# Performance work log

Measured on AMD Instinct MI355X. Metric: run time of the kernel, lower is better.

Reference implementation:

```python
import jax, jax.numpy as jnp
import numpy as np

B, T, C, H = 4, 4096, 1024, 128

def setup_inputs() -> dict:
    key = jax.random.key(0)
    k1, k2, k3, k4 = jax.random.split(key, 4)
    x = jax.random.normal(k1, (B, T, C), dtype=jnp.float32)
    # nn.Linear(embed, head, bias=False): y = x @ W, store W as [C, H]
    s = 1.0 / np.sqrt(C)
    Wk = jax.random.normal(k2, (C, H), dtype=jnp.float32) * s
    Wq = jax.random.normal(k3, (C, H), dtype=jnp.float32) * s
    Wv = jax.random.normal(k4, (C, H), dtype=jnp.float32) * s
    return {"x": x, "Wk": Wk, "Wq": Wq, "Wv": Wv}

def reference(x, Wk, Wq, Wv):
    Bx, Tx, Cx = x.shape
    scale = Wk.shape[1] ** -0.5
    k = x @ Wk  # [B,T,H]
    q = x @ Wq
    v = x @ Wv
    att = jnp.einsum('bth,bsh->bts', q, k) * scale  # [B,T,T]
    causal = jnp.triu(jnp.ones((Tx, Tx), dtype=bool), k=1)
    att = jnp.where(causal, -jnp.inf, att)
    att = jax.nn.softmax(att, axis=-1)
    # dropout is identity in eval mode
    out = jnp.einsum('bts,bsh->bth', att, v)  # [B,T,H]
    return out
```

## Files before the change

kernel.cpp:

```cpp
#include <hip/hip_runtime.h>
#include <stdint.h>
#include <math.h>

#define B_ 4
#define T_ 4096
#define C_ 1024
#define H_ 128

typedef __attribute__((ext_vector_type(8))) short s16x8;
typedef __attribute__((ext_vector_type(4))) float f32x4;

__device__ __forceinline__ unsigned short f2bf(float f) {
    union { float f; unsigned u; } v; v.f = f;
    unsigned r = v.u + 0x7fffu + ((v.u >> 16) & 1u);
    return (unsigned short)(r >> 16);
}

__device__ __forceinline__ s16x8 as_frag(uint4 u) {
    union { uint4 u; s16x8 s; } v; v.u = u; return v.s;
}

#define QSC (0.0883883476f * 1.4426950408f)

__global__ __launch_bounds__(256) void k_wt(const float* __restrict__ Wk,
                                            const float* __restrict__ Wq,
                                            const float* __restrict__ Wv,
                                            unsigned short* __restrict__ Wt) {
    __shared__ float tile[64][65];
    int w = blockIdx.z;
    const float* W = (w == 0) ? Wk : (w == 1) ? Wq : Wv;
    int c0 = blockIdx.x * 64, h0 = blockIdx.y * 64;
    int tid = threadIdx.x;
#pragma unroll
    for (int k = 0; k < 16; k++) {
        int idx = tid + k * 256;
        int r = idx >> 6, c = idx & 63;
        tile[r][c] = W[(size_t)(c0 + r) * H_ + h0 + c];
    }
    __syncthreads();
#pragma unroll
    for (int k = 0; k < 16; k++) {
        int idx = tid + k * 256;
        int hh = idx >> 6, cc = idx & 63;
        Wt[(size_t)(w * H_ + h0 + hh) * C_ + c0 + cc] = f2bf(tile[cc][hh]);
    }
}

__global__ __launch_bounds__(256, 3) void k_qkv(const float* __restrict__ x,
                                                const unsigned short* __restrict__ Wt,
                                                unsigned short* __restrict__ Qb,
                                                unsigned short* __restrict__ Kb,
                                                unsigned short* __restrict__ Vt) {
    __shared__ unsigned short a_lds[2][64 * 72];
    int tid = threadIdx.x;
    int wv = tid >> 6, lane = tid & 63, quad = lane >> 4, lo = lane & 15;
    int r0 = blockIdx.x * 64;
    int cb = blockIdx.y;
    int nt0 = wv * 3;

    f32x4 acc[3][4];
#pragma unroll
    for (int i = 0; i < 3; i++)
#pragma unroll
        for (int j = 0; j < 4; j++) acc[i][j] = (f32x4){0.f, 0.f, 0.f, 0.f};

    const int row_s = tid >> 2;
    const int seg_s = (tid & 3) * 16;
    size_t xbase = (size_t)(r0 + row_s) * C_ + seg_s;

    const unsigned short* wp[3];
#pragma unroll
    for (int nt = 0; nt < 3; nt++)
        wp[nt] = Wt + (size_t)(cb * 192 + (nt0 + nt) * 16 + lo) * C_ + quad * 8;

    auto pack_store = [&](unsigned short* buf, const float4 (&f)[4]) {
        uint4 u0, u1;
        u0.x = (unsigned)f2bf(f[0].x) | ((unsigned)f2bf(f[0].y) << 16);
        u0.y = (unsigned)f2bf(f[0].z) | ((unsigned)f2bf(f[0].w) << 16);
        u0.z = (unsigned)f2bf(f[1].x) | ((unsigned)f2bf(f[1].y) << 16);
        u0.w = (unsigned)f2bf(f[1].z) | ((unsigned)f2bf(f[1].w) << 16);
        u1.x = (unsigned)f2bf(f[2].x) | ((unsigned)f2bf(f[2].y) << 16);
        u1.y = (unsigned)f2bf(f[2].z) | ((unsigned)f2bf(f[2].w) << 16);
        u1.z = (unsigned)f2bf(f[3].x) | ((unsigned)f2bf(f[3].y) << 16);
        u1.w = (unsigned)f2bf(f[3].z) | ((unsigned)f2bf(f[3].w) << 16);
        *(uint4*)&buf[row_s * 72 + seg_s] = u0;
        *(uint4*)&buf[row_s * 72 + seg_s + 8] = u1;
    };
    auto load_x = [&](float4 (&f)[4], int kc) {
        const float* xp = x + xbase + kc * 64;
#pragma unroll
        for (int j = 0; j < 4; j++) f[j] = *(const float4*)(xp + j * 4);
    };

    float4 xr[4];
    load_x(xr, 0);
    pack_store(a_lds[0], xr);
    __syncthreads();

    for (int kc = 0; kc < 16; kc++) {
        const unsigned short* buf = a_lds[kc & 1];
        float4 xn[4];
        if (kc < 15) load_x(xn, kc + 1);
        s16x8 b[3][2];
#pragma unroll
        for (int nt = 0; nt < 3; nt++)
#pragma unroll
            for (int kh = 0; kh < 2; kh++)
                b[nt][kh] = *(const s16x8*)(wp[nt] + kc * 64 + kh * 32);
        s16x8 af[4][2];
#pragma unroll
        for (int mt = 0; mt < 4; mt++)
#pragma unroll
            for (int kh = 0; kh < 2; kh++)
                af[mt][kh] = *(const s16x8*)&buf[(mt * 16 + lo) * 72 + kh * 32 + quad * 8];
#pragma unroll
        for (int nt = 0; nt < 3; nt++)
#pragma unroll
            for (int kh = 0; kh < 2; kh++)
#pragma unroll
                for (int mt = 0; mt < 4; mt++)
                    acc[nt][mt] = __builtin_amdgcn_mfma_f32_16x16x32_bf16(
                        af[mt][kh], b[nt][kh], acc[nt][mt], 0, 0, 0);
        if (kc < 15) pack_store((unsigned short*)a_lds[(kc & 1) ^ 1], xn);
        __syncthreads();
    }

#pragma unroll
    for (int nt = 0; nt < 3; nt++) {
        int col = cb * 192 + (nt0 + nt) * 16 + lo;
        int w = col >> 7, h = col & 127;
#pragma unroll
        for (int mt = 0; mt < 4; mt++) {
            int mrow = r0 + mt * 16 + quad * 4;
            if (w == 2) {
                int b = mrow >> 12, t0 = mrow & 4095;
                int tp = (t0 & ~31) + (((t0 & 15) >> 2) << 3) + (((t0 >> 4) & 1) << 2);
                uint2 pk;
                pk.x = (unsigned)f2bf(acc[nt][mt][0]) | ((unsigned)f2bf(acc[nt][mt][1]) << 16);
                pk.y = (unsigned)f2bf(acc[nt][mt][2]) | ((unsigned)f2bf(acc[nt][mt][3]) << 16);
                *(uint2*)(Vt + (size_t)(b * H_ + h) * T_ + tp) = pk;
            } else if (w == 1) {
                unsigned short* dst = Qb + (size_t)mrow * H_ + h;
#pragma unroll
                for (int r = 0; r < 4; r++)
                    dst[(size_t)r * H_] = f2bf(acc[nt][mt][r] * QSC);
            } else {
                unsigned short* dst = Kb + (size_t)mrow * H_ + h;
#pragma unroll
                for (int r = 0; r < 4; r++)
                    dst[(size_t)r * H_] = f2bf(acc[nt][mt][r]);
            }
        }
    }
}

#define LOAD_KV(kv0)                                                            \
    do {                                                                        \
        const uint4* kg = (const uint4*)(Kb + (size_t)(batch * T_ + (kv0) + srow_k) * H_); \
        pk0 = kg[sseg_k + 0]; pk1 = kg[sseg_k + 1];                             \
        pk2 = kg[sseg_k + 2]; pk3 = kg[sseg_k + 3];                             \
        const uint4* vg = (const uint4*)(Vt + (size_t)(batch * H_ + srow_v) * T_ + (kv0)); \
        pv0 = vg[sseg_v + 0]; pv1 = vg[sseg_v + 1];                             \
        pv2 = vg[sseg_v + 2]; pv3 = vg[sseg_v + 3];                             \
    } while (0)

template <int NSPLIT>
__global__ __launch_bounds__(256, 3) void k_attn(const unsigned short* __restrict__ Qb,
                                                 const unsigned short* __restrict__ Kb,
                                                 const unsigned short* __restrict__ Vt,
                                                 float* __restrict__ Opart,
                                                 float* __restrict__ Mpart,
                                                 float* __restrict__ Lpart,
                                                 float* __restrict__ out) {
    __shared__ uint4 kbuf[64 * 16];
    __shared__ uint4 vbuf[128 * 8];

    int tid = threadIdx.x;
    int wv = tid >> 6, lane = tid & 63, quad = lane >> 4, lo = lane & 15;

    int id = blockIdx.x;
    int qt = 63 - id / (4 * NSPLIT);
    int rem = id % (4 * NSPLIT);
    int batch = rem / NSPLIT;
    int split = rem % NSPLIT;
    int m0 = qt * 64 + wv * 16;
    int query = m0 + lo;

    s16x8 qf[4];
    size_t qrow = (size_t)(batch * T_ + m0 + lo) * H_;
#pragma unroll
    for (int ks = 0; ks < 4; ks++)
        qf[ks] = *(const s16x8*)(Qb + qrow + ks * 32 + quad * 8);

    f32x4 acc_o[8];
#pragma unroll
    for (int o = 0; o < 8; o++) acc_o[o] = (f32x4){0.f, 0.f, 0.f, 0.f};
    float m_i = -INFINITY, l_i = 0.f;

    const int srow_k = tid >> 2, sseg_k = (tid & 3) * 4;
    const int srow_v = tid >> 1, sseg_v = (tid & 1) * 4;

    uint4 pk0, pk1, pk2, pk3, pv0, pv1, pv2, pv3;
    if (split <= qt) LOAD_KV(split * 64);

    for (int t = split; t <= qt; t += NSPLIT) {
        int kv0 = t * 64;
        kbuf[srow_k * 16 + ((sseg_k + 0) ^ (srow_k & 15))] = pk0;
        kbuf[srow_k * 16 + ((sseg_k + 1) ^ (srow_k & 15))] = pk1;
        kbuf[srow_k * 16 + ((sseg_k + 2) ^ (srow_k & 15))] = pk2;
        kbuf[srow_k * 16 + ((sseg_k + 3) ^ (srow_k & 15))] = pk3;
        vbuf[srow_v * 8 + ((sseg_v + 0) ^ (srow_v & 7))] = pv0;
        vbuf[srow_v * 8 + ((sseg_v + 1) ^ (srow_v & 7))] = pv1;
        vbuf[srow_v * 8 + ((sseg_v + 2) ^ (srow_v & 7))] = pv2;
        vbuf[srow_v * 8 + ((sseg_v + 3) ^ (srow_v & 7))] = pv3;
        __syncthreads();
        if (t + NSPLIT <= qt) LOAD_KV((t + NSPLIT) * 64);

        f32x4 s_acc[4];
#pragma unroll
        for (int nt = 0; nt < 4; nt++) s_acc[nt] = (f32x4){0.f, 0.f, 0.f, 0.f};
#pragma unroll
        for (int ks = 0; ks < 4; ks++) {
#pragma unroll
            for (int nt = 0; nt < 4; nt++) {
                s16x8 kf = as_frag(kbuf[(nt * 16 + lo) * 16 + ((ks * 4 + quad) ^ lo)]);
                s_acc[nt] = __builtin_amdgcn_mfma_f32_16x16x32_bf16(kf, qf[ks], s_acc[nt], 0, 0, 0);
            }
        }

        float p[4][4];
        bool diag = (t == qt);
#pragma unroll
        for (int nt = 0; nt < 4; nt++)
#pragma unroll
            for (int r = 0; r < 4; r++) {
                float sv = s_acc[nt][r];
                if (diag && (kv0 + nt * 16 + quad * 4 + r > query)) sv = -INFINITY;
                p[nt][r] = sv;
            }

        float mx = p[0][0];
#pragma unroll
        for (int nt = 0; nt < 4; nt++)
#pragma unroll
            for (int r = 0; r < 4; r++) mx = fmaxf(mx, p[nt][r]);
        mx = fmaxf(mx, __shfl_xor(mx, 16));
        mx = fmaxf(mx, __shfl_xor(mx, 32));
        float mnew = fmaxf(m_i, mx);
        if (__any(mnew > m_i)) {
            float alpha = exp2f(m_i - mnew);
            l_i *= alpha;
            m_i = mnew;
#pragma unroll
            for (int o = 0; o < 8; o++)
#pragma unroll
                for (int r = 0; r < 4; r++) acc_o[o][r] *= alpha;
        }
        float rs = 0.f;
#pragma unroll
        for (int nt = 0; nt < 4; nt++)
#pragma unroll
            for (int r = 0; r < 4; r++) {
                float pv = exp2f(p[nt][r] - mnew);
                p[nt][r] = pv;
                rs += pv;
            }
        rs += __shfl_xor(rs, 16);
        rs += __shfl_xor(rs, 32);
        l_i += rs;

        s16x8 pf[2];
#pragma unroll
        for (int kt = 0; kt < 2; kt++) {
            uint4 u;
            u.x = (__float_as_uint(p[2 * kt][0]) >> 16) | ((__float_as_uint(p[2 * kt][1]) >> 16) << 16);
            u.y = (__float_as_uint(p[2 * kt][2]) >> 16) | ((__float_as_uint(p[2 * kt][3]) >> 16) << 16);
            u.z = (__float_as_uint(p[2 * kt + 1][0]) >> 16) | ((__float_as_uint(p[2 * kt + 1][1]) >> 16) << 16);
            u.w = (__float_as_uint(p[2 * kt + 1][2]) >> 16) | ((__float_as_uint(p[2 * kt + 1][3]) >> 16) << 16);
            pf[kt] = as_frag(u);
        }

#pragma unroll
        for (int kt = 0; kt < 2; kt++)
#pragma unroll
            for (int o = 0; o < 8; o++) {
                int vrow = o * 16 + lo;
                s16x8 vf = as_frag(vbuf[vrow * 8 + ((kt * 4 + quad) ^ (vrow & 7))]);
                acc_o[o] = __builtin_amdgcn_mfma_f32_16x16x32_bf16(vf, pf[kt], acc_o[o], 0, 0, 0);
            }
        __syncthreads();
    }

    int rowg = batch * T_ + m0 + lo;
    if (NSPLIT == 1) {
        float inv = 1.0f / l_i;
#pragma unroll
        for (int o = 0; o < 8; o++) {
            float4 v = {acc_o[o][0] * inv, acc_o[o][1] * inv,
                        acc_o[o][2] * inv, acc_o[o][3] * inv};
            *(float4*)(out + (size_t)rowg * H_ + o * 16 + quad * 4) = v;
        }
    } else {
        float* Op = Opart + (size_t)split * (16384 * 128);
#pragma unroll
        for (int o = 0; o < 8; o++) {
            float4 v = {acc_o[o][0], acc_o[o][1], acc_o[o][2], acc_o[o][3]};
            *(float4*)(Op + (size_t)rowg * H_ + o * 16 + quad * 4) = v;
        }
        if (quad == 0) {
            Mpart[split * 16384 + rowg] = m_i;
            Lpart[split * 16384 + rowg] = l_i;
        }
    }
}

template <int NSPLIT>
__global__ __launch_bounds__(256) void k_comb(const float* __restrict__ Opart,
                                              const float* __restrict__ Mpart,
                                              const float* __restrict__ Lpart,
                                              float* __restrict__ out) {
    int tid = threadIdx.x;
    int row = blockIdx.x * 8 + (tid >> 5);
    int h4 = (tid & 31) * 4;
    float m[NSPLIT], l[NSPLIT];
    float M = -INFINITY;
#pragma unroll
    for (int s = 0; s < NSPLIT; s++) {
        m[s] = Mpart[s * 16384 + row];
        l[s] = Lpart[s * 16384 + row];
        M = fmaxf(M, m[s]);
    }
    float4 o = {0.f, 0.f, 0.f, 0.f};
    float den = 0.f;
#pragma unroll
    for (int s = 0; s < NSPLIT; s++) {
        float w = exp2f(m[s] - M);
        den += w * l[s];
        float4 v = *(const float4*)(Opart + ((size_t)s * 16384 + row) * H_ + h4);
        o.x += w * v.x; o.y += w * v.y; o.z += w * v.z; o.w += w * v.w;
    }
    float inv = 1.0f / den;
    float4 r = {o.x * inv, o.y * inv, o.z * inv, o.w * inv};
    *(float4*)(out + (size_t)row * H_ + h4) = r;
}

extern "C" void kernel_launch(void* const* d_in, const int* in_sizes, int n_in,
                              void* d_out, int out_size, void* d_ws, size_t ws_size,
                              hipStream_t stream) {
    const float* x  = (const float*)d_in[0];
    const float* Wk = (const float*)d_in[1];
    const float* Wq = (const float*)d_in[2];
    const float* Wv = (const float*)d_in[3];
    char* ws = (char*)d_ws;
    unsigned short* Wt = (unsigned short*)ws;
    unsigned short* Qb = (unsigned short*)(ws + (1u << 20));
    unsigned short* Kb = (unsigned short*)(ws + (5u << 20));
    unsigned short* Vt = (unsigned short*)(ws + (9u << 20));
    float* out = (float*)d_out;

    const size_t SPLIT_O = (size_t)16384 * 128 * 4;
    const size_t base = (size_t)13 << 20;
    const size_t need4 = base + 4 * SPLIT_O + 8 * 65536;
    const size_t need2 = base + 2 * SPLIT_O + 4 * 65536;

    k_wt  <<<dim3(16, 2, 3), 256, 0, stream>>>(Wk, Wq, Wv, Wt);
    k_qkv <<<dim3(256, 2), 256, 0, stream>>>(x, Wt, Qb, Kb, Vt);

    if (ws_size >= need4) {
        float* Op = (float*)(ws + base);
        float* Mp = (float*)(ws + base + 4 * SPLIT_O);
        float* Lp = (float*)(ws + base + 4 * SPLIT_O + 4 * 65536);
        k_attn<4><<<1024, 256, 0, stream>>>(Qb, Kb, Vt, Op, Mp, Lp, out);
        k_comb<4><<<2048, 256, 0, stream>>>(Op, Mp, Lp, out);
    } else if (ws_size >= need2) {
        float* Op = (float*)(ws + base);
        float* Mp = (float*)(ws + base + 2 * SPLIT_O);
        float* Lp = (float*)(ws + base + 2 * SPLIT_O + 2 * 65536);
        k_attn<2><<<512, 256, 0, stream>>>(Qb, Kb, Vt, Op, Mp, Lp, out);
        k_comb<2><<<2048, 256, 0, stream>>>(Op, Mp, Lp, out);
    } else {
        k_attn<1><<<256, 256, 0, stream>>>(Qb, Kb, Vt, nullptr, nullptr, nullptr, out);
    }
}
```

Before: 168.0 us.

## Split causal attention into contiguous KV chunks, lazy rescale, retile QKV projection

Attention work is now split into contiguous chunks of at most CH key tiles per query tile, replacing the strided NSPLIT split. This balances block work across the causal triangle, and the combine kernel merges a variable number of partials per row. The online softmax now rescales only when the row max grows by more than 8 (log2 units) and defers the cross-lane row-sum reduction to the end, which cuts shuffles and rescale work per tile. The QKV projection uses 512-thread blocks over 32 rows covering all 384 columns, with a two-stage unrolled double buffer. The trade-offs are larger partial workspace and combine traffic, and the lazy rescale threshold could in principle affect numerical range.

```diff
diff --git a/kernel.cpp b/kernel.cpp
--- a/kernel.cpp
+++ b/kernel.cpp
@@ -18,6 +18,11 @@
 
 __device__ __forceinline__ s16x8 as_frag(uint4 u) {
     union { uint4 u; s16x8 s; } v; v.u = u; return v.s;
+}
+
+__host__ __device__ constexpr int chunks_total(int CH) {
+    int a = 64 / CH, b = 64 % CH;
+    return CH * a * (a + 1) / 2 + b * (a + 1);
 }
 
 #define QSC (0.0883883476f * 1.4426950408f)
@@ -46,70 +51,50 @@
     }
 }
 
-__global__ __launch_bounds__(256, 3) void k_qkv(const float* __restrict__ x,
+__global__ __launch_bounds__(512, 4) void k_qkv(const float* __restrict__ x,
                                                 const unsigned short* __restrict__ Wt,
                                                 unsigned short* __restrict__ Qb,
                                                 unsigned short* __restrict__ Kb,
                                                 unsigned short* __restrict__ Vt) {
-    __shared__ unsigned short a_lds[2][64 * 72];
+    __shared__ unsigned short a_lds[2][32 * 72];
     int tid = threadIdx.x;
     int wv = tid >> 6, lane = tid & 63, quad = lane >> 4, lo = lane & 15;
-    int r0 = blockIdx.x * 64;
-    int cb = blockIdx.y;
-    int nt0 = wv * 3;
-
-    f32x4 acc[3][4];
+    int r0 = blockIdx.x * 32;
+
+    f32x4 acc[3][2];
 #pragma unroll
     for (int i = 0; i < 3; i++)
 #pragma unroll
-        for (int j = 0; j < 4; j++) acc[i][j] = (f32x4){0.f, 0.f, 0.f, 0.f};
-
-    const int row_s = tid >> 2;
-    const int seg_s = (tid & 3) * 16;
+        for (int j = 0; j < 2; j++) acc[i][j] = (f32x4){0.f, 0.f, 0.f, 0.f};
+
+    const int row_s = tid >> 4;
+    const int seg_s = (tid & 15) * 4;
     size_t xbase = (size_t)(r0 + row_s) * C_ + seg_s;
 
     const unsigned short* wp[3];
 #pragma unroll
     for (int nt = 0; nt < 3; nt++)
-        wp[nt] = Wt + (size_t)(cb * 192 + (nt0 + nt) * 16 + lo) * C_ + quad * 8;
-
-    auto pack_store = [&](unsigned short* buf, const float4 (&f)[4]) {
-        uint4 u0, u1;
-        u0.x = (unsigned)f2bf(f[0].x) | ((unsigned)f2bf(f[0].y) << 16);
-        u0.y = (unsigned)f2bf(f[0].z) | ((unsigned)f2bf(f[0].w) << 16);
-        u0.z = (unsigned)f2bf(f[1].x) | ((unsigned)f2bf(f[1].y) << 16);
-        u0.w = (unsigned)f2bf(f[1].z) | ((unsigned)f2bf(f[1].w) << 16);
-        u1.x = (unsigned)f2bf(f[2].x) | ((unsigned)f2bf(f[2].y) << 16);
-        u1.y = (unsigned)f2bf(f[2].z) | ((unsigned)f2bf(f[2].w) << 16);
-        u1.z = (unsigned)f2bf(f[3].x) | ((unsigned)f2bf(f[3].y) << 16);
-        u1.w = (unsigned)f2bf(f[3].z) | ((unsigned)f2bf(f[3].w) << 16);
-        *(uint4*)&buf[row_s * 72 + seg_s] = u0;
-        *(uint4*)&buf[row_s * 72 + seg_s + 8] = u1;
+        wp[nt] = Wt + (size_t)((wv * 3 + nt) * 16 + lo) * C_ + quad * 8;
+
+    auto load_x = [&](int kc) -> float4 {
+        return *(const float4*)(x + xbase + kc * 64);
     };
-    auto load_x = [&](float4 (&f)[4], int kc) {
-        const float* xp = x + xbase + kc * 64;
-#pragma unroll
-        for (int j = 0; j < 4; j++) f[j] = *(const float4*)(xp + j * 4);
+    auto pack_store = [&](unsigned short* buf, float4 f) {
+        uint2 u;
+        u.x = (unsigned)f2bf(f.x) | ((unsigned)f2bf(f.y) << 16);
+        u.y = (unsigned)f2bf(f.z) | ((unsigned)f2bf(f.w) << 16);
+        *(uint2*)&buf[row_s * 72 + seg_s] = u;
     };
-
-    float4 xr[4];
-    load_x(xr, 0);
-    pack_store(a_lds[0], xr);
-    __syncthreads();
-
-    for (int kc = 0; kc < 16; kc++) {
-        const unsigned short* buf = a_lds[kc & 1];
-        float4 xn[4];
-        if (kc < 15) load_x(xn, kc + 1);
+    auto compute = [&](const unsigned short* buf, int kc) {
         s16x8 b[3][2];
 #pragma unroll
         for (int nt = 0; nt < 3; nt++)
 #pragma unroll
             for (int kh = 0; kh < 2; kh++)
                 b[nt][kh] = *(const s16x8*)(wp[nt] + kc * 64 + kh * 32);
-        s16x8 af[4][2];
-#pragma unroll
-        for (int mt = 0; mt < 4; mt++)
+        s16x8 af[2][2];
+#pragma unroll
+        for (int mt = 0; mt < 2; mt++)
 #pragma unroll
             for (int kh = 0; kh < 2; kh++)
                 af[mt][kh] = *(const s16x8*)&buf[(mt * 16 + lo) * 72 + kh * 32 + quad * 8];
@@ -118,19 +103,34 @@
 #pragma unroll
             for (int kh = 0; kh < 2; kh++)
 #pragma unroll
-                for (int mt = 0; mt < 4; mt++)
+                for (int mt = 0; mt < 2; mt++)
                     acc[nt][mt] = __builtin_amdgcn_mfma_f32_16x16x32_bf16(
                         af[mt][kh], b[nt][kh], acc[nt][mt], 0, 0, 0);
-        if (kc < 15) pack_store((unsigned short*)a_lds[(kc & 1) ^ 1], xn);
+    };
+
+    float4 p0 = load_x(0);
+    float4 p1 = load_x(1);
+    pack_store(a_lds[0], p0);
+    __syncthreads();
+
+    for (int kc2 = 0; kc2 < 8; kc2++) {
+        int kc = kc2 * 2;
+        if (kc + 2 < 16) p0 = load_x(kc + 2);
+        compute(a_lds[0], kc);
+        pack_store(a_lds[1], p1);
         __syncthreads();
+        if (kc + 3 < 16) p1 = load_x(kc + 3);
+        compute(a_lds[1], kc + 1);
+        if (kc + 2 < 16) pack_store(a_lds[0], p0);
+        __syncthreads();
     }
 
 #pragma unroll
     for (int nt = 0; nt < 3; nt++) {
-        int col = cb * 192 + (nt0 + nt) * 16 + lo;
+        int col = (wv * 3 + nt) * 16 + lo;
         int w = col >> 7, h = col & 127;
 #pragma unroll
-        for (int mt = 0; mt < 4; mt++) {
+        for (int mt = 0; mt < 2; mt++) {
             int mrow = r0 + mt * 16 + quad * 4;
             if (w == 2) {
                 int b = mrow >> 12, t0 = mrow & 4095;
@@ -164,7 +164,7 @@
         pv2 = vg[sseg_v + 2]; pv3 = vg[sseg_v + 3];                             \
     } while (0)
 
-template <int NSPLIT>
+template <int CH>
 __global__ __launch_bounds__(256, 3) void k_attn(const unsigned short* __restrict__ Qb,
                                                  const unsigned short* __restrict__ Kb,
                                                  const unsigned short* __restrict__ Vt,
@@ -179,10 +179,18 @@
     int wv = tid >> 6, lane = tid & 63, quad = lane >> 4, lo = lane & 15;
 
     int id = blockIdx.x;
-    int qt = 63 - id / (4 * NSPLIT);
-    int rem = id % (4 * NSPLIT);
-    int batch = rem / NSPLIT;
-    int split = rem % NSPLIT;
+    int qt, batch, tbeg, tend, slot = 0;
+    if constexpr (CH > 0) {
+        slot = id >> 2; batch = id & 3;
+        int s = slot, q = 63;
+        for (;;) { int nc = (q + CH) / CH; if (s < nc) break; s -= nc; --q; }
+        qt = q;
+        tbeg = s * CH;
+        tend = min(tbeg + CH, qt + 1);
+    } else {
+        qt = 63 - (id >> 2); batch = id & 3;
+        tbeg = 0; tend = qt + 1;
+    }
     int m0 = qt * 64 + wv * 16;
     int query = m0 + lo;
 
@@ -201,9 +209,9 @@
     const int srow_v = tid >> 1, sseg_v = (tid & 1) * 4;
 
     uint4 pk0, pk1, pk2, pk3, pv0, pv1, pv2, pv3;
-    if (split <= qt) LOAD_KV(split * 64);
-
-    for (int t = split; t <= qt; t += NSPLIT) {
+    LOAD_KV(tbeg * 64);
+
+    for (int t = tbeg; t < tend; ++t) {
         int kv0 = t * 64;
         kbuf[srow_k * 16 + ((sseg_k + 0) ^ (srow_k & 15))] = pk0;
         kbuf[srow_k * 16 + ((sseg_k + 1) ^ (srow_k & 15))] = pk1;
@@ -214,7 +222,7 @@
         vbuf[srow_v * 8 + ((sseg_v + 2) ^ (srow_v & 7))] = pv2;
         vbuf[srow_v * 8 + ((sseg_v + 3) ^ (srow_v & 7))] = pv3;
         __syncthreads();
-        if (t + NSPLIT <= qt) LOAD_KV((t + NSPLIT) * 64);
+        if (t + 1 < tend) LOAD_KV((t + 1) * 64);
 
         f32x4 s_acc[4];
 #pragma unroll
@@ -244,10 +252,10 @@
         for (int nt = 0; nt < 4; nt++)
 #pragma unroll
             for (int r = 0; r < 4; r++) mx = fmaxf(mx, p[nt][r]);
-        mx = fmaxf(mx, __shfl_xor(mx, 16));
-        mx = fmaxf(mx, __shfl_xor(mx, 32));
-        float mnew = fmaxf(m_i, mx);
-        if (__any(mnew > m_i)) {
+        if (__any(mx > m_i + 8.0f)) {
+            float rm = fmaxf(mx, __shfl_xor(mx, 16));
+            rm = fmaxf(rm, __shfl_xor(rm, 32));
+            float mnew = fmaxf(m_i, rm);
             float alpha = exp2f(m_i - mnew);
             l_i *= alpha;
             m_i = mnew;
@@ -261,12 +269,10 @@
         for (int nt = 0; nt < 4; nt++)
 #pragma unroll
             for (int r = 0; r < 4; r++) {
-                float pv = exp2f(p[nt][r] - mnew);
+                float pv = exp2f(p[nt][r] - m_i);
                 p[nt][r] = pv;
                 rs += pv;
             }
-        rs += __shfl_xor(rs, 16);
-        rs += __shfl_xor(rs, 32);
         l_i += rs;
 
         s16x8 pf[2];
@@ -291,53 +297,60 @@
         __syncthreads();
     }
 
-    int rowg = batch * T_ + m0 + lo;
-    if (NSPLIT == 1) {
+    l_i += __shfl_xor(l_i, 16);
+    l_i += __shfl_xor(l_i, 32);
+
+    if constexpr (CH > 0) {
+        constexpr int NCH = chunks_total(CH);
+        size_t pr = (size_t)(batch * NCH + slot) * 64 + wv * 16 + lo;
+        float* Op = Opart + pr * 128;
+#pragma unroll
+        for (int o = 0; o < 8; o++) {
+            float4 v = {acc_o[o][0], acc_o[o][1], acc_o[o][2], acc_o[o][3]};
+            *(float4*)(Op + o * 16 + quad * 4) = v;
+        }
+        if (quad == 0) { Mpart[pr] = m_i; Lpart[pr] = l_i; }
+    } else {
         float inv = 1.0f / l_i;
+        int rowg = batch * T_ + m0 + lo;
 #pragma unroll
         for (int o = 0; o < 8; o++) {
             float4 v = {acc_o[o][0] * inv, acc_o[o][1] * inv,
                         acc_o[o][2] * inv, acc_o[o][3] * inv};
             *(float4*)(out + (size_t)rowg * H_ + o * 16 + quad * 4) = v;
         }
-    } else {
-        float* Op = Opart + (size_t)split * (16384 * 128);
-#pragma unroll
-        for (int o = 0; o < 8; o++) {
-            float4 v = {acc_o[o][0], acc_o[o][1], acc_o[o][2], acc_o[o][3]};
-            *(float4*)(Op + (size_t)rowg * H_ + o * 16 + quad * 4) = v;
-        }
-        if (quad == 0) {
-            Mpart[split * 16384 + rowg] = m_i;
-            Lpart[split * 16384 + rowg] = l_i;
-        }
-    }
-}
-
-template <int NSPLIT>
+    }
+}
+
+template <int CH>
 __global__ __launch_bounds__(256) void k_comb(const float* __restrict__ Opart,
                                               const float* __restrict__ Mpart,
                                               const float* __restrict__ Lpart,
                                               float* __restrict__ out) {
+    constexpr int NCH = chunks_total(CH);
     int tid = threadIdx.x;
     int row = blockIdx.x * 8 + (tid >> 5);
     int h4 = (tid & 31) * 4;
-    float m[NSPLIT], l[NSPLIT];
-    float M = -INFINITY;
-#pragma unroll
-    for (int s = 0; s < NSPLIT; s++) {
-        m[s] = Mpart[s * 16384 + row];
-        l[s] = Lpart[s * 16384 + row];
-        M = fmaxf(M, m[s]);
-    }
+    int batch = row >> 12, t = row & 4095, qt = t >> 6;
+    int n = qt + 1;
+    int nc = (qt + CH) / CH;
+    int a = n / CH, b = n % CH;
+    int S = CH * a * (a + 1) / 2 + b * (a + 1);
+    int base = NCH - S;
+    float M = -INFINITY, den = 0.f;
     float4 o = {0.f, 0.f, 0.f, 0.f};
-    float den = 0.f;
-#pragma unroll
-    for (int s = 0; s < NSPLIT; s++) {
-        float w = exp2f(m[s] - M);
-        den += w * l[s];
-        float4 v = *(const float4*)(Opart + ((size_t)s * 16384 + row) * H_ + h4);
-        o.x += w * v.x; o.y += w * v.y; o.z += w * v.z; o.w += w * v.w;
+    for (int s = 0; s < nc; ++s) {
+        size_t pr = (size_t)(batch * NCH + base + s) * 64 + (t & 63);
+        float ms = Mpart[pr], ls = Lpart[pr];
+        float4 v = *(const float4*)(Opart + pr * 128 + h4);
+        float Mn = fmaxf(M, ms);
+        float wa = exp2f(M - Mn), wb = exp2f(ms - Mn);
+        den = den * wa + ls * wb;
+        o.x = o.x * wa + v.x * wb;
+        o.y = o.y * wa + v.y * wb;
+        o.z = o.z * wa + v.z * wb;
+        o.w = o.w * wa + v.w * wb;
+        M = Mn;
     }
     float inv = 1.0f / den;
     float4 r = {o.x * inv, o.y * inv, o.z * inv, o.w * inv};
@@ -358,27 +371,29 @@
     unsigned short* Vt = (unsigned short*)(ws + (9u << 20));
     float* out = (float*)d_out;
 
-    const size_t SPLIT_O = (size_t)16384 * 128 * 4;
     const size_t base = (size_t)13 << 20;
-    const size_t need4 = base + 4 * SPLIT_O + 8 * 65536;
-    const size_t need2 = base + 2 * SPLIT_O + 4 * 65536;
+    constexpr int NCH10 = chunks_total(10);
+    constexpr int NCH21 = chunks_total(21);
+    auto need_for = [&](int nch) {
+        return base + (size_t)4 * nch * 64 * (128 * 4) + 2 * (size_t)4 * nch * 64 * 4;
+    };
 
     k_wt  <<<dim3(16, 2, 3), 256, 0, stream>>>(Wk, Wq, Wv, Wt);
-    k_qkv <<<dim3(256, 2), 256, 0, stream>>>(x, Wt, Qb, Kb, Vt);
-
-    if (ws_size >= need4) {
+    k_qkv <<<dim3(512), 512, 0, stream>>>(x, Wt, Qb, Kb, Vt);
+
+    if (ws_size >= need_for(NCH10)) {
         float* Op = (float*)(ws + base);
-        float* Mp = (float*)(ws + base + 4 * SPLIT_O);
-        float* Lp = (float*)(ws + base + 4 * SPLIT_O + 4 * 65536);
-        k_attn<4><<<1024, 256, 0, stream>>>(Qb, Kb, Vt, Op, Mp, Lp, out);
-        k_comb<4><<<2048, 256, 0, stream>>>(Op, Mp, Lp, out);
-    } else if (ws_size >= need2) {
+        float* Mp = Op + (size_t)4 * NCH10 * 64 * 128;
+        float* Lp = Mp + (size_t)4 * NCH10 * 64;
+        k_attn<10><<<4 * NCH10, 256, 0, stream>>>(Qb, Kb, Vt, Op, Mp, Lp, out);
+        k_comb<10><<<2048, 256, 0, stream>>>(Op, Mp, Lp, out);
+    } else if (ws_size >= need_for(NCH21)) {
         float* Op = (float*)(ws + base);
-        float* Mp = (float*)(ws + base + 2 * SPLIT_O);
-        float* Lp = (float*)(ws + base + 2 * SPLIT_O + 2 * 65536);
-        k_attn<2><<<512, 256, 0, stream>>>(Qb, Kb, Vt, Op, Mp, Lp, out);
-        k_comb<2><<<2048, 256, 0, stream>>>(Op, Mp, Lp, out);
+        float* Mp = Op + (size_t)4 * NCH21 * 64 * 128;
+        float* Lp = Mp + (size_t)4 * NCH21 * 64;
+        k_attn<21><<<4 * NCH21, 256, 0, stream>>>(Qb, Kb, Vt, Op, Mp, Lp, out);
+        k_comb<21><<<2048, 256, 0, stream>>>(Op, Mp, Lp, out);
     } else {
-        k_attn<1><<<256, 256, 0, stream>>>(Qb, Kb, Vt, nullptr, nullptr, nullptr, out);
-    }
-}
+        k_attn<0><<<256, 256, 0, stream>>>(Qb, Kb, Vt, nullptr, nullptr, nullptr, out);
+    }
+}
```

New measurement: 190.6 us. +13.5%, slower.
